# Kernel tuning notes

Hardware: AMD Instinct MI355X
Metric: run time of the kernel (lower is better)

Reference implementation:

```python
import jax, jax.numpy as jnp
import numpy as np

BN_EPS = 1e-3  # keras BatchNormalization default epsilon


def _bn(h, gamma, beta, mean, var):
    # inference-mode batchnorm over last (feature) axis
    return (h - mean) * (gamma / jnp.sqrt(var + BN_EPS)) + beta


def _gcn(x, adj, W, b):
    # GCNConv: relu(A @ X @ W + b); contract features first (cheaper), then propagate
    return jax.nn.relu(jnp.einsum('bnm,bmh->bnh', adj, x @ W) + b)


def setup_inputs() -> dict:
    key = jax.random.key(0)
    ks = jax.random.split(key, 20)
    B, N, F = 4, 4096, 64
    H, O = 64, 64
    d = {
        'x': jax.random.normal(ks[0], (B, N, F), dtype=jnp.float32),
        'adj': jax.random.uniform(ks[1], (B, N, N), dtype=jnp.float32) / N,
    }
    dims = [(F, H), (H, H), (H, O)]
    for i, (din, dout) in enumerate(dims, start=1):
        k1, k2 = jax.random.split(ks[1 + i], 2)
        d[f'W{i}'] = jax.random.normal(k1, (din, dout), dtype=jnp.float32) / np.sqrt(din)
        d[f'b{i}'] = jnp.zeros((dout,), dtype=jnp.float32)
        d[f'g{i}'] = jnp.ones((dout,), dtype=jnp.float32)
        d[f'be{i}'] = jnp.zeros((dout,), dtype=jnp.float32)
        d[f'm{i}'] = 0.1 * jax.random.normal(ks[6 + i], (dout,), dtype=jnp.float32)
        d[f'v{i}'] = jnp.ones((dout,), dtype=jnp.float32) + 0.1 * jax.random.uniform(ks[10 + i], (dout,), dtype=jnp.float32)
    d['Wl'] = jax.random.normal(ks[15], (H + H + O, O), dtype=jnp.float32) / np.sqrt(H + H + O)
    d['bl'] = jnp.zeros((O,), dtype=jnp.float32)
    return d


def reference(x, adj, W1, b1, g1, be1, m1, v1, W2, b2, g2, be2, m2, v2,
              W3, b3, g3, be3, m3, v3, Wl, bl):
    x1 = _bn(_gcn(x, adj, W1, b1), g1, be1, m1, v1)   # [B,N,H]
    x2 = _bn(_gcn(x1, adj, W2, b2), g2, be2, m2, v2)  # [B,N,H]
    x3 = _bn(_gcn(x2, adj, W3, b3), g3, be3, m3, v3)  # [B,N,O]
    h = jnp.concatenate([x1, x2, x3], axis=-1)        # [B,N,2H+O]
    return jax.nn.relu(h @ Wl + bl)                   # [B,N,O]
```

## Files before the change

kernel.cpp:

```cpp
#include <hip/hip_runtime.h>

typedef __attribute__((ext_vector_type(8))) short short8;
typedef __attribute__((ext_vector_type(4))) float f32x4;
typedef __attribute__((ext_vector_type(2))) unsigned u32x2;

#define NN 4096
#define BN_EPS 1e-3f

__device__ inline unsigned short f2bf(float f) {
    unsigned u = __builtin_bit_cast(unsigned, f);
    return (unsigned short)((u + 0x7fffu + ((u >> 16) & 1u)) >> 16);
}
__device__ inline float bf2f(unsigned short h) {
    return __builtin_bit_cast(float, ((unsigned)h) << 16);
}
__device__ inline short8 pk8(f32x4 f0, f32x4 f1) {
    short8 B;
    B[0] = (short)f2bf(f0.x); B[1] = (short)f2bf(f0.y);
    B[2] = (short)f2bf(f0.z); B[3] = (short)f2bf(f0.w);
    B[4] = (short)f2bf(f1.x); B[5] = (short)f2bf(f1.y);
    B[6] = (short)f2bf(f1.z); B[7] = (short)f2bf(f1.w);
    return B;
}

__global__ __launch_bounds__(256) void n72_gcn(
    const float* __restrict__ adj, const unsigned short* __restrict__ tT,
    const float* __restrict__ bias, const float* __restrict__ gamma,
    const float* __restrict__ beta, const float* __restrict__ mean,
    const float* __restrict__ var, unsigned short* __restrict__ xout)
{
    const int tid = threadIdx.x;
    const int s = tid >> 6, lane = tid & 63;
    const int rl = lane & 15, grp = lane >> 4;
    const int bid = blockIdx.x;
    const int b = bid >> 7, rb = bid & 127;
    const int row32 = rb * 32;

    const float* arow0 = adj + ((long)b * NN + row32 + rl) * (long)NN;
    const float* arow1 = arow0 + 16 * (long)NN;
    const unsigned short* t0 = tT + ((long)b * 64 + rl) * (long)NN;
    const unsigned short* t1 = t0 + 16 * (long)NN;
    const unsigned short* t2 = t0 + 32 * (long)NN;
    const unsigned short* t3 = t0 + 48 * (long)NN;
    const int m0 = s * 1024 + grp * 8;

    f32x4 p0 = {}, p1 = {}, p2 = {}, p3 = {};
    f32x4 q0 = {}, q1 = {}, q2 = {}, q3 = {};

    for (int it = 0; it < 32; ++it) {
        const int m = m0 + it * 32;
        short8 A0 = *(const short8*)(t0 + m);
        short8 A1 = *(const short8*)(t1 + m);
        short8 A2 = *(const short8*)(t2 + m);
        short8 A3 = *(const short8*)(t3 + m);
        f32x4 f0 = *(const f32x4*)(arow0 + m);
        f32x4 f1 = *(const f32x4*)(arow0 + m + 4);
        f32x4 g0 = *(const f32x4*)(arow1 + m);
        f32x4 g1 = *(const f32x4*)(arow1 + m + 4);
        short8 B0 = pk8(f0, f1);
        short8 B1 = pk8(g0, g1);
        p0 = __builtin_amdgcn_mfma_f32_16x16x32_bf16(A0, B0, p0, 0, 0, 0);
        p1 = __builtin_amdgcn_mfma_f32_16x16x32_bf16(A1, B0, p1, 0, 0, 0);
        p2 = __builtin_amdgcn_mfma_f32_16x16x32_bf16(A2, B0, p2, 0, 0, 0);
        p3 = __builtin_amdgcn_mfma_f32_16x16x32_bf16(A3, B0, p3, 0, 0, 0);
        q0 = __builtin_amdgcn_mfma_f32_16x16x32_bf16(A0, B1, q0, 0, 0, 0);
        q1 = __builtin_amdgcn_mfma_f32_16x16x32_bf16(A1, B1, q1, 0, 0, 0);
        q2 = __builtin_amdgcn_mfma_f32_16x16x32_bf16(A2, B1, q2, 0, 0, 0);
        q3 = __builtin_amdgcn_mfma_f32_16x16x32_bf16(A3, B1, q3, 0, 0, 0);
    }

    __shared__ float red[4][2][16][68];
    *(f32x4*)&red[s][0][rl][ 0 + grp * 4] = p0;
    *(f32x4*)&red[s][0][rl][16 + grp * 4] = p1;
    *(f32x4*)&red[s][0][rl][32 + grp * 4] = p2;
    *(f32x4*)&red[s][0][rl][48 + grp * 4] = p3;
    *(f32x4*)&red[s][1][rl][ 0 + grp * 4] = q0;
    *(f32x4*)&red[s][1][rl][16 + grp * 4] = q1;
    *(f32x4*)&red[s][1][rl][32 + grp * 4] = q2;
    *(f32x4*)&red[s][1][rl][48 + grp * 4] = q3;
    __syncthreads();

    const int r2 = tid >> 4, cq = (tid & 15) * 4;
    f32x4 bi = *(const f32x4*)(bias + cq);
    f32x4 mn = *(const f32x4*)(mean + cq);
    f32x4 vr = *(const f32x4*)(var + cq);
    f32x4 gm = *(const f32x4*)(gamma + cq);
    f32x4 bt = *(const f32x4*)(beta + cq);
    f32x4 sc;
    for (int q = 0; q < 4; ++q) sc[q] = gm[q] / sqrtf(vr[q] + BN_EPS);

    for (int rg = 0; rg < 2; ++rg) {
        f32x4 v = *(const f32x4*)&red[0][rg][r2][cq];
        v += *(const f32x4*)&red[1][rg][r2][cq];
        v += *(const f32x4*)&red[2][rg][r2][cq];
        v += *(const f32x4*)&red[3][rg][r2][cq];
        float o[4];
        for (int q = 0; q < 4; ++q) {
            float h = v[q] + bi[q];
            h = h > 0.f ? h : 0.f;
            o[q] = (h - mn[q]) * sc[q] + bt[q];
        }
        u32x2 o2;
        o2.x = (unsigned)f2bf(o[0]) | ((unsigned)f2bf(o[1]) << 16);
        o2.y = (unsigned)f2bf(o[2]) | ((unsigned)f2bf(o[3]) << 16);
        *(u32x2*)(xout + ((long)b * NN + row32 + rg * 16 + r2) * 64 + cq) = o2;
    }
}

__global__ __launch_bounds__(256) void h72_feat32(
    const float* __restrict__ xin, const float* __restrict__ W,
    unsigned short* __restrict__ tT)
{
    __shared__ float xs[64][68];
    __shared__ float Ws[64][68];
    const int tid = threadIdx.x;
    const int bid = blockIdx.x;
    const int b = bid >> 6, nb = bid & 63;
    {
        const int rr = tid >> 2, kq = (tid & 3) * 16;
        const float* xp = xin + ((long)b * NN + nb * 64 + rr) * 64 + kq;
        const float* wp = W + rr * 64 + kq;
        for (int j = 0; j < 4; ++j) {
            *(f32x4*)&xs[rr][kq + j * 4] = *(const f32x4*)(xp + j * 4);
            *(f32x4*)&Ws[rr][kq + j * 4] = *(const f32x4*)(wp + j * 4);
        }
    }
    __syncthreads();
    const int c = tid >> 2, n0 = (tid & 3) * 16;
    float outv[16];
    for (int j = 0; j < 16; ++j) outv[j] = 0.f;
    for (int kt = 0; kt < 4; ++kt) {
        float wc[16];
#pragma unroll
        for (int kk = 0; kk < 16; ++kk) wc[kk] = Ws[kt * 16 + kk][c];
#pragma unroll
        for (int j = 0; j < 16; ++j)
#pragma unroll
            for (int kk = 0; kk < 16; ++kk)
                outv[j] += xs[n0 + j][kt * 16 + kk] * wc[kk];
    }
    unsigned short* tp = tT + ((long)b * 64 + c) * (long)NN + nb * 64 + n0;
#pragma unroll
    for (int j = 0; j < 16; j += 2)
        *(unsigned*)(tp + j) =
            (unsigned)f2bf(outv[j]) | ((unsigned)f2bf(outv[j + 1]) << 16);
}

__global__ __launch_bounds__(256) void h72_featbf(
    const unsigned short* __restrict__ xin, const float* __restrict__ W,
    unsigned short* __restrict__ tT)
{
    __shared__ float xs[64][68];
    __shared__ float Ws[64][68];
    const int tid = threadIdx.x;
    const int bid = blockIdx.x;
    const int b = bid >> 6, nb = bid & 63;
    {
        const int rr = tid >> 2, kq = (tid & 3) * 16;
        const unsigned short* xp = xin + ((long)b * NN + nb * 64 + rr) * 64 + kq;
        const float* wp = W + rr * 64 + kq;
        short8 v0 = *(const short8*)(xp);
        short8 v1 = *(const short8*)(xp + 8);
        for (int j = 0; j < 8; ++j) {
            xs[rr][kq + j]     = bf2f((unsigned short)v0[j]);
            xs[rr][kq + 8 + j] = bf2f((unsigned short)v1[j]);
        }
        for (int j = 0; j < 4; ++j)
            *(f32x4*)&Ws[rr][kq + j * 4] = *(const f32x4*)(wp + j * 4);
    }
    __syncthreads();
    const int c = tid >> 2, n0 = (tid & 3) * 16;
    float outv[16];
    for (int j = 0; j < 16; ++j) outv[j] = 0.f;
    for (int kt = 0; kt < 4; ++kt) {
        float wc[16];
#pragma unroll
        for (int kk = 0; kk < 16; ++kk) wc[kk] = Ws[kt * 16 + kk][c];
#pragma unroll
        for (int j = 0; j < 16; ++j)
#pragma unroll
            for (int kk = 0; kk < 16; ++kk)
                outv[j] += xs[n0 + j][kt * 16 + kk] * wc[kk];
    }
    unsigned short* tp = tT + ((long)b * 64 + c) * (long)NN + nb * 64 + n0;
#pragma unroll
    for (int j = 0; j < 16; j += 2)
        *(unsigned*)(tp + j) =
            (unsigned)f2bf(outv[j]) | ((unsigned)f2bf(outv[j + 1]) << 16);
}

__global__ __launch_bounds__(256) void h72_mlp(
    const unsigned short* __restrict__ x1, const unsigned short* __restrict__ x2,
    const unsigned short* __restrict__ x3, const float* __restrict__ Wl,
    const float* __restrict__ bl, float* __restrict__ out)
{
    __shared__ float hs[64][196];
    const int tid = threadIdx.x;
    const int bid = blockIdx.x;
    const int b = bid >> 6, nb = bid & 63;
    {
        const int rr = tid >> 2, kq = (tid & 3) * 16;
        const long base = ((long)b * NN + nb * 64 + rr) * 64 + kq;
        short8 u0 = *(const short8*)(x1 + base);
        short8 u1 = *(const short8*)(x1 + base + 8);
        short8 v0 = *(const short8*)(x2 + base);
        short8 v1 = *(const short8*)(x2 + base + 8);
        short8 w0 = *(const short8*)(x3 + base);
        short8 w1 = *(const short8*)(x3 + base + 8);
        for (int j = 0; j < 8; ++j) {
            hs[rr][  0 + kq + j]     = bf2f((unsigned short)u0[j]);
            hs[rr][  0 + kq + 8 + j] = bf2f((unsigned short)u1[j]);
            hs[rr][ 64 + kq + j]     = bf2f((unsigned short)v0[j]);
            hs[rr][ 64 + kq + 8 + j] = bf2f((unsigned short)v1[j]);
            hs[rr][128 + kq + j]     = bf2f((unsigned short)w0[j]);
            hs[rr][128 + kq + 8 + j] = bf2f((unsigned short)w1[j]);
        }
    }
    __syncthreads();
    const int c = tid >> 2, n0 = (tid & 3) * 16;
    float acc[16];
    const float blc = bl[c];
    for (int j = 0; j < 16; ++j) acc[j] = blc;
    for (int kt = 0; kt < 12; ++kt) {
        float wc[16];
#pragma unroll
        for (int kk = 0; kk < 16; ++kk) wc[kk] = Wl[(kt * 16 + kk) * 64 + c];
#pragma unroll
        for (int j = 0; j < 16; ++j)
#pragma unroll
            for (int kk = 0; kk < 16; ++kk)
                acc[j] += hs[n0 + j][kt * 16 + kk] * wc[kk];
    }
    float* op = out + ((long)b * NN + nb * 64 + n0) * 64 + c;
#pragma unroll
    for (int j = 0; j < 16; ++j) {
        float v2 = acc[j] > 0.f ? acc[j] : 0.f;
        op[j * 64] = v2;
    }
}

extern "C" void kernel_launch(void* const* d_in, const int* in_sizes, int n_in,
                              void* d_out, int out_size, void* d_ws, size_t ws_size,
                              hipStream_t stream)
{
    (void)in_sizes; (void)n_in; (void)out_size; (void)ws_size;
    const float* x   = (const float*)d_in[0];
    const float* adj = (const float*)d_in[1];
    const float* W1  = (const float*)d_in[2];
    const float* b1  = (const float*)d_in[3];
    const float* g1  = (const float*)d_in[4];
    const float* be1 = (const float*)d_in[5];
    const float* m1  = (const float*)d_in[6];
    const float* v1  = (const float*)d_in[7];
    const float* W2  = (const float*)d_in[8];
    const float* b2  = (const float*)d_in[9];
    const float* g2  = (const float*)d_in[10];
    const float* be2 = (const float*)d_in[11];
    const float* m2  = (const float*)d_in[12];
    const float* v2  = (const float*)d_in[13];
    const float* W3  = (const float*)d_in[14];
    const float* b3  = (const float*)d_in[15];
    const float* g3  = (const float*)d_in[16];
    const float* be3 = (const float*)d_in[17];
    const float* m3  = (const float*)d_in[18];
    const float* v3  = (const float*)d_in[19];
    const float* Wl  = (const float*)d_in[20];
    const float* bl  = (const float*)d_in[21];

    float* out = (float*)d_out;
    unsigned short* tT = (unsigned short*)(out + 524288);

    char* ws = (char*)d_ws;
    unsigned short* x1 = (unsigned short*)(ws);
    unsigned short* x2 = (unsigned short*)(ws + 2097152);
    unsigned short* x3 = (unsigned short*)(ws + 4194304);

    h72_feat32<<<256, 256, 0, stream>>>(x, W1, tT);
    n72_gcn<<<512, 256, 0, stream>>>(adj, tT, b1, g1, be1, m1, v1, x1);

    h72_featbf<<<256, 256, 0, stream>>>(x1, W2, tT);
    n72_gcn<<<512, 256, 0, stream>>>(adj, tT, b2, g2, be2, m2, v2, x2);

    h72_featbf<<<256, 256, 0, stream>>>(x2, W3, tT);
    n72_gcn<<<512, 256, 0, stream>>>(adj, tT, b3, g3, be3, m3, v3, x3);

    h72_mlp<<<256, 256, 0, stream>>>(x1, x2, x3, Wl, bl, out);
}
```

Measured before the change: 268.7 us.

## Cache bf16 copy of adjacency in first GCN pass and reuse in later layers

The first GCN layer now converts the fp32 adjacency tiles to bf16 as it streams them and writes that copy to workspace. Layers two and three read the half-size bf16 adjacency instead of the fp32 original, which cuts the dominant HBM traffic in those passes. The cost is an extra 128 MB write in layer one and a dependence on a large workspace, with a fallback to the old path when the workspace is too small. Numerics are unchanged because the old kernel already rounded adjacency to bf16 before the MFMA.

```diff
diff --git a/kernel.cpp b/kernel.cpp
--- a/kernel.cpp
+++ b/kernel.cpp
@@ -21,6 +21,176 @@
     B[4] = (short)f2bf(f1.x); B[5] = (short)f2bf(f1.y);
     B[6] = (short)f2bf(f1.z); B[7] = (short)f2bf(f1.w);
     return B;
+}
+
+__global__ __launch_bounds__(256) void n72_gcns(
+    const float* __restrict__ adj, const unsigned short* __restrict__ tT,
+    unsigned short* __restrict__ adj_bf,
+    const float* __restrict__ bias, const float* __restrict__ gamma,
+    const float* __restrict__ beta, const float* __restrict__ mean,
+    const float* __restrict__ var, unsigned short* __restrict__ xout)
+{
+    const int tid = threadIdx.x;
+    const int s = tid >> 6, lane = tid & 63;
+    const int rl = lane & 15, grp = lane >> 4;
+    const int bid = blockIdx.x;
+    const int b = bid >> 7, rb = bid & 127;
+    const int row32 = rb * 32;
+    const long aoff = ((long)b * NN + row32 + rl) * (long)NN;
+
+    const float* arow0 = adj + aoff;
+    const float* arow1 = arow0 + 16 * (long)NN;
+    unsigned short* srow0 = adj_bf + aoff;
+    unsigned short* srow1 = srow0 + 16 * (long)NN;
+    const unsigned short* t0 = tT + ((long)b * 64 + rl) * (long)NN;
+    const unsigned short* t1 = t0 + 16 * (long)NN;
+    const unsigned short* t2 = t0 + 32 * (long)NN;
+    const unsigned short* t3 = t0 + 48 * (long)NN;
+    const int m0 = s * 1024 + grp * 8;
+
+    f32x4 p0 = {}, p1 = {}, p2 = {}, p3 = {};
+    f32x4 q0 = {}, q1 = {}, q2 = {}, q3 = {};
+
+    for (int it = 0; it < 32; ++it) {
+        const int m = m0 + it * 32;
+        short8 A0 = *(const short8*)(t0 + m);
+        short8 A1 = *(const short8*)(t1 + m);
+        short8 A2 = *(const short8*)(t2 + m);
+        short8 A3 = *(const short8*)(t3 + m);
+        f32x4 f0 = *(const f32x4*)(arow0 + m);
+        f32x4 f1 = *(const f32x4*)(arow0 + m + 4);
+        f32x4 g0 = *(const f32x4*)(arow1 + m);
+        f32x4 g1 = *(const f32x4*)(arow1 + m + 4);
+        short8 B0 = pk8(f0, f1);
+        short8 B1 = pk8(g0, g1);
+        *(short8*)(srow0 + m) = B0;
+        *(short8*)(srow1 + m) = B1;
+        p0 = __builtin_amdgcn_mfma_f32_16x16x32_bf16(A0, B0, p0, 0, 0, 0);
+        p1 = __builtin_amdgcn_mfma_f32_16x16x32_bf16(A1, B0, p1, 0, 0, 0);
+        p2 = __builtin_amdgcn_mfma_f32_16x16x32_bf16(A2, B0, p2, 0, 0, 0);
+        p3 = __builtin_amdgcn_mfma_f32_16x16x32_bf16(A3, B0, p3, 0, 0, 0);
+        q0 = __builtin_amdgcn_mfma_f32_16x16x32_bf16(A0, B1, q0, 0, 0, 0);
+        q1 = __builtin_amdgcn_mfma_f32_16x16x32_bf16(A1, B1, q1, 0, 0, 0);
+        q2 = __builtin_amdgcn_mfma_f32_16x16x32_bf16(A2, B1, q2, 0, 0, 0);
+        q3 = __builtin_amdgcn_mfma_f32_16x16x32_bf16(A3, B1, q3, 0, 0, 0);
+    }
+
+    __shared__ float red[4][2][16][68];
+    *(f32x4*)&red[s][0][rl][ 0 + grp * 4] = p0;
+    *(f32x4*)&red[s][0][rl][16 + grp * 4] = p1;
+    *(f32x4*)&red[s][0][rl][32 + grp * 4] = p2;
+    *(f32x4*)&red[s][0][rl][48 + grp * 4] = p3;
+    *(f32x4*)&red[s][1][rl][ 0 + grp * 4] = q0;
+    *(f32x4*)&red[s][1][rl][16 + grp * 4] = q1;
+    *(f32x4*)&red[s][1][rl][32 + grp * 4] = q2;
+    *(f32x4*)&red[s][1][rl][48 + grp * 4] = q3;
+    __syncthreads();
+
+    const int r2 = tid >> 4, cq = (tid & 15) * 4;
+    f32x4 bi = *(const f32x4*)(bias + cq);
+    f32x4 mn = *(const f32x4*)(mean + cq);
+    f32x4 vr = *(const f32x4*)(var + cq);
+    f32x4 gm = *(const f32x4*)(gamma + cq);
+    f32x4 bt = *(const f32x4*)(beta + cq);
+    f32x4 sc;
+    for (int q = 0; q < 4; ++q) sc[q] = gm[q] / sqrtf(vr[q] + BN_EPS);
+
+    for (int rg = 0; rg < 2; ++rg) {
+        f32x4 v = *(const f32x4*)&red[0][rg][r2][cq];
+        v += *(const f32x4*)&red[1][rg][r2][cq];
+        v += *(const f32x4*)&red[2][rg][r2][cq];
+        v += *(const f32x4*)&red[3][rg][r2][cq];
+        float o[4];
+        for (int q = 0; q < 4; ++q) {
+            float h = v[q] + bi[q];
+            h = h > 0.f ? h : 0.f;
+            o[q] = (h - mn[q]) * sc[q] + bt[q];
+        }
+        u32x2 o2;
+        o2.x = (unsigned)f2bf(o[0]) | ((unsigned)f2bf(o[1]) << 16);
+        o2.y = (unsigned)f2bf(o[2]) | ((unsigned)f2bf(o[3]) << 16);
+        *(u32x2*)(xout + ((long)b * NN + row32 + rg * 16 + r2) * 64 + cq) = o2;
+    }
+}
+
+__global__ __launch_bounds__(256) void n72_gcnb(
+    const unsigned short* __restrict__ adj, const unsigned short* __restrict__ tT,
+    const float* __restrict__ bias, const float* __restrict__ gamma,
+    const float* __restrict__ beta, const float* __restrict__ mean,
+    const float* __restrict__ var, unsigned short* __restrict__ xout)
+{
+    const int tid = threadIdx.x;
+    const int s = tid >> 6, lane = tid & 63;
+    const int rl = lane & 15, grp = lane >> 4;
+    const int bid = blockIdx.x;
+    const int b = bid >> 7, rb = bid & 127;
+    const int row32 = rb * 32;
+
+    const unsigned short* arow0 = adj + ((long)b * NN + row32 + rl) * (long)NN;
+    const unsigned short* arow1 = arow0 + 16 * (long)NN;
+    const unsigned short* t0 = tT + ((long)b * 64 + rl) * (long)NN;
+    const unsigned short* t1 = t0 + 16 * (long)NN;
+    const unsigned short* t2 = t0 + 32 * (long)NN;
+    const unsigned short* t3 = t0 + 48 * (long)NN;
+    const int m0 = s * 1024 + grp * 8;
+
+    f32x4 p0 = {}, p1 = {}, p2 = {}, p3 = {};
+    f32x4 q0 = {}, q1 = {}, q2 = {}, q3 = {};
+
+    for (int it = 0; it < 32; ++it) {
+        const int m = m0 + it * 32;
+        short8 A0 = *(const short8*)(t0 + m);
+        short8 A1 = *(const short8*)(t1 + m);
+        short8 A2 = *(const short8*)(t2 + m);
+        short8 A3 = *(const short8*)(t3 + m);
+        short8 B0 = *(const short8*)(arow0 + m);
+        short8 B1 = *(const short8*)(arow1 + m);
+        p0 = __builtin_amdgcn_mfma_f32_16x16x32_bf16(A0, B0, p0, 0, 0, 0);
+        p1 = __builtin_amdgcn_mfma_f32_16x16x32_bf16(A1, B0, p1, 0, 0, 0);
+        p2 = __builtin_amdgcn_mfma_f32_16x16x32_bf16(A2, B0, p2, 0, 0, 0);
+        p3 = __builtin_amdgcn_mfma_f32_16x16x32_bf16(A3, B0, p3, 0, 0, 0);
+        q0 = __builtin_amdgcn_mfma_f32_16x16x32_bf16(A0, B1, q0, 0, 0, 0);
+        q1 = __builtin_amdgcn_mfma_f32_16x16x32_bf16(A1, B1, q1, 0, 0, 0);
+        q2 = __builtin_amdgcn_mfma_f32_16x16x32_bf16(A2, B1, q2, 0, 0, 0);
+        q3 = __builtin_amdgcn_mfma_f32_16x16x32_bf16(A3, B1, q3, 0, 0, 0);
+    }
+
+    __shared__ float red[4][2][16][68];
+    *(f32x4*)&red[s][0][rl][ 0 + grp * 4] = p0;
+    *(f32x4*)&red[s][0][rl][16 + grp * 4] = p1;
+    *(f32x4*)&red[s][0][rl][32 + grp * 4] = p2;
+    *(f32x4*)&red[s][0][rl][48 + grp * 4] = p3;
+    *(f32x4*)&red[s][1][rl][ 0 + grp * 4] = q0;
+    *(f32x4*)&red[s][1][rl][16 + grp * 4] = q1;
+    *(f32x4*)&red[s][1][rl][32 + grp * 4] = q2;
+    *(f32x4*)&red[s][1][rl][48 + grp * 4] = q3;
+    __syncthreads();
+
+    const int r2 = tid >> 4, cq = (tid & 15) * 4;
+    f32x4 bi = *(const f32x4*)(bias + cq);
+    f32x4 mn = *(const f32x4*)(mean + cq);
+    f32x4 vr = *(const f32x4*)(var + cq);
+    f32x4 gm = *(const f32x4*)(gamma + cq);
+    f32x4 bt = *(const f32x4*)(beta + cq);
+    f32x4 sc;
+    for (int q = 0; q < 4; ++q) sc[q] = gm[q] / sqrtf(vr[q] + BN_EPS);
+
+    for (int rg = 0; rg < 2; ++rg) {
+        f32x4 v = *(const f32x4*)&red[0][rg][r2][cq];
+        v += *(const f32x4*)&red[1][rg][r2][cq];
+        v += *(const f32x4*)&red[2][rg][r2][cq];
+        v += *(const f32x4*)&red[3][rg][r2][cq];
+        float o[4];
+        for (int q = 0; q < 4; ++q) {
+            float h = v[q] + bi[q];
+            h = h > 0.f ? h : 0.f;
+            o[q] = (h - mn[q]) * sc[q] + bt[q];
+        }
+        u32x2 o2;
+        o2.x = (unsigned)f2bf(o[0]) | ((unsigned)f2bf(o[1]) << 16);
+        o2.y = (unsigned)f2bf(o[2]) | ((unsigned)f2bf(o[3]) << 16);
+        *(u32x2*)(xout + ((long)b * NN + row32 + rg * 16 + r2) * 64 + cq) = o2;
+    }
 }
 
 __global__ __launch_bounds__(256) void n72_gcn(
@@ -243,7 +413,7 @@
                               void* d_out, int out_size, void* d_ws, size_t ws_size,
                               hipStream_t stream)
 {
-    (void)in_sizes; (void)n_in; (void)out_size; (void)ws_size;
+    (void)in_sizes; (void)n_in; (void)out_size;
     const float* x   = (const float*)d_in[0];
     const float* adj = (const float*)d_in[1];
     const float* W1  = (const float*)d_in[2];
@@ -274,15 +444,30 @@
     unsigned short* x1 = (unsigned short*)(ws);
     unsigned short* x2 = (unsigned short*)(ws + 2097152);
     unsigned short* x3 = (unsigned short*)(ws + 4194304);
-
-    h72_feat32<<<256, 256, 0, stream>>>(x, W1, tT);
-    n72_gcn<<<512, 256, 0, stream>>>(adj, tT, b1, g1, be1, m1, v1, x1);
-
-    h72_featbf<<<256, 256, 0, stream>>>(x1, W2, tT);
-    n72_gcn<<<512, 256, 0, stream>>>(adj, tT, b2, g2, be2, m2, v2, x2);
-
-    h72_featbf<<<256, 256, 0, stream>>>(x2, W3, tT);
-    n72_gcn<<<512, 256, 0, stream>>>(adj, tT, b3, g3, be3, m3, v3, x3);
-
-    h72_mlp<<<256, 256, 0, stream>>>(x1, x2, x3, Wl, bl, out);
-}
+    unsigned short* adjbf = (unsigned short*)(ws + 6291456);
+    const size_t NEED_BIG = 6291456 + (size_t)4 * NN * NN * 2;
+
+    if (ws_size >= NEED_BIG) {
+        h72_feat32<<<256, 256, 0, stream>>>(x, W1, tT);
+        n72_gcns<<<512, 256, 0, stream>>>(adj, tT, adjbf, b1, g1, be1, m1, v1, x1);
+
+        h72_featbf<<<256, 256, 0, stream>>>(x1, W2, tT);
+        n72_gcnb<<<512, 256, 0, stream>>>(adjbf, tT, b2, g2, be2, m2, v2, x2);
+
+        h72_featbf<<<256, 256, 0, stream>>>(x2, W3, tT);
+        n72_gcnb<<<512, 256, 0, stream>>>(adjbf, tT, b3, g3, be3, m3, v3, x3);
+
+        h72_mlp<<<256, 256, 0, stream>>>(x1, x2, x3, Wl, bl, out);
+    } else {
+        h72_feat32<<<256, 256, 0, stream>>>(x, W1, tT);
+        n72_gcn<<<512, 256, 0, stream>>>(adj, tT, b1, g1, be1, m1, v1, x1);
+
+        h72_featbf<<<256, 256, 0, stream>>>(x1, W2, tT);
+        n72_gcn<<<512, 256, 0, stream>>>(adj, tT, b2, g2, be2, m2, v2, x2);
+
+        h72_featbf<<<256, 256, 0, stream>>>(x2, W3, tT);
+        n72_gcn<<<512, 256, 0, stream>>>(adj, tT, b3, g3, be3, m3, v3, x3);
+
+        h72_mlp<<<256, 256, 0, stream>>>(x1, x2, x3, Wl, bl, out);
+    }
+}
```

After: 294.7 us. 1.1x slower.
